# Kernel optimization log

Measured on AMD Instinct MI355X. Metric: run time of the kernel, lower is better.

## Reference

```python
import jax, jax.numpy as jnp
import numpy as np

C = 384
NH = 8        # LocalCrossAttention heads
CA_NH = 2     # inner CrossAttention heads
D_WIN = 6
SIGMA = D_WIN / 2.0
EPS = 1e-6


def _ln(x, g, b):
    mu = jnp.mean(x, axis=-1, keepdims=True)
    var = jnp.mean((x - mu) ** 2, axis=-1, keepdims=True)
    return (x - mu) / jnp.sqrt(var + EPS) * g + b


def _cross_attn(qx, kvx, Wq, Wkv, Wp, bp, nh):
    B, QN, c = qx.shape
    N = kvx.shape[1]
    hd = c // nh
    scale = hd ** -0.5
    qh = (qx @ Wq).reshape(B, QN, nh, hd).transpose(0, 2, 1, 3) * scale  # bhqd
    kvh = (kvx @ Wkv).reshape(B, N, 2, nh, hd).transpose(2, 0, 3, 1, 4)
    k, v = kvh[0], kvh[1]                                               # bhkd
    attn = jax.nn.softmax(jnp.einsum('bhqd,bhkd->bhqk', qh, k), axis=-1)
    x = jnp.einsum('bhqk,bhkd->bhqd', attn, v).transpose(0, 2, 1, 3).reshape(B, QN, c)
    return x @ Wp + bp


def _forward(q, kv, Wq, Wkv, Wproj, bproj, Wp_w, Wp_b, vp_w, vp_b, qpos_w, qpos_b,
             ca1_Wq, ca1_Wkv, ca1_Wproj, ca1_bproj,
             ca2_Wq, ca2_Wkv, ca2_Wproj, ca2_bproj,
             lnq1_g, lnq1_b, lnkv1_g, lnkv1_b, lnq2_g, lnq2_b, lnkv2_g, lnkv2_b, H, W):
    bs, QN, c = q.shape
    N = kv.shape[1]
    hd = c // NH
    scale = hd ** -0.5

    # main q/k/v
    qh = (q @ Wq).reshape(bs, QN, NH, hd).transpose(0, 2, 1, 3) * scale   # [bs,NH,QN,hd]
    kvh = (kv @ Wkv).reshape(bs, N, 2, NH, hd).transpose(2, 0, 3, 1, 4)
    k, v = kvh[0], kvh[1]                                                 # [bs,NH,N,hd]

    # position prediction branch
    q_for_pos = jnp.tile(q, (1, H, 1))                                    # [bs,QN*H,C]
    p = q_for_pos @ qpos_w + qpos_b
    p = _cross_attn(_ln(p, lnq1_g, lnq1_b), _ln(q_for_pos, lnkv1_g, lnkv1_b),
                    ca1_Wq, ca1_Wkv, ca1_Wproj, ca1_bproj, CA_NH)
    p = _cross_attn(_ln(p, lnq2_g, lnq2_b), _ln(kv, lnkv2_g, lnkv2_b),
                    ca2_Wq, ca2_Wkv, ca2_Wproj, ca2_bproj, CA_NH)
    p_t = jax.nn.sigmoid(jnp.tanh(p @ Wp_w + Wp_b) @ vp_w + vp_b) * W     # [bs,QN*H,1]

    # Gaussian window over W columns, broadcast over heads
    idx = jnp.arange(W, dtype=q.dtype)                                    # [W]
    gauss = jnp.exp(-((idx[None, :] - p_t) ** 2) / (2.0 * SIGMA ** 2))    # [bs,QN*H,W]
    gauss = gauss[:, None]                                                # [bs,1,QN*H,W]

    attn = jnp.einsum('bhqd,bhkd->bhqk', qh, k)                           # [bs,NH,QN,N]
    attn = attn.reshape(bs, NH, QN * H, W) * gauss
    attn = attn.reshape(bs, NH, QN, N)
    attn = jax.nn.softmax(attn, axis=-1)

    x = jnp.einsum('bhqk,bhkd->bhqd', attn, v).transpose(0, 2, 1, 3).reshape(bs, QN, c)
    return x @ Wproj + bproj


def setup_inputs() -> dict:
    key = jax.random.key(0)
    ks = jax.random.split(key, 16)
    s = 0.05
    d = {
        'q': jax.random.normal(ks[0], (32, 64, C), jnp.float32),
        'kv': jax.random.normal(ks[1], (32, 1024, C), jnp.float32),
        'Wq': jax.random.normal(ks[2], (C, C), jnp.float32) * s,
        'Wkv': jax.random.normal(ks[3], (C, 2 * C), jnp.float32) * s,
        'Wproj': jax.random.normal(ks[4], (C, C), jnp.float32) * s,
        'bproj': jnp.zeros((C,), jnp.float32),
        'Wp_w': jax.random.normal(ks[5], (C, C), jnp.float32) * s,
        'Wp_b': jnp.zeros((C,), jnp.float32),
        'vp_w': jax.random.normal(ks[6], (C, 1), jnp.float32) * s,
        'vp_b': jnp.zeros((1,), jnp.float32),
        'qpos_w': jax.random.normal(ks[7], (C, C), jnp.float32) * s,
        'qpos_b': jnp.zeros((C,), jnp.float32),
        'ca1_Wq': jax.random.normal(ks[8], (C, C), jnp.float32) * s,
        'ca1_Wkv': jax.random.normal(ks[9], (C, 2 * C), jnp.float32) * s,
        'ca1_Wproj': jax.random.normal(ks[10], (C, C), jnp.float32) * s,
        'ca1_bproj': jnp.zeros((C,), jnp.float32),
        'ca2_Wq': jax.random.normal(ks[11], (C, C), jnp.float32) * s,
        'ca2_Wkv': jax.random.normal(ks[12], (C, 2 * C), jnp.float32) * s,
        'ca2_Wproj': jax.random.normal(ks[13], (C, C), jnp.float32) * s,
        'ca2_bproj': jnp.zeros((C,), jnp.float32),
        'lnq1_g': jnp.ones((C,), jnp.float32), 'lnq1_b': jnp.zeros((C,), jnp.float32),
        'lnkv1_g': jnp.ones((C,), jnp.float32), 'lnkv1_b': jnp.zeros((C,), jnp.float32),
        'lnq2_g': jnp.ones((C,), jnp.float32), 'lnq2_b': jnp.zeros((C,), jnp.float32),
        'lnkv2_g': jnp.ones((C,), jnp.float32), 'lnkv2_b': jnp.zeros((C,), jnp.float32),
        'H': 8,
        'W': 128,
    }
    return d


def reference(q, kv, Wq, Wkv, Wproj, bproj, Wp_w, Wp_b, vp_w, vp_b, qpos_w, qpos_b,
              ca1_Wq, ca1_Wkv, ca1_Wproj, ca1_bproj,
              ca2_Wq, ca2_Wkv, ca2_Wproj, ca2_bproj,
              lnq1_g, lnq1_b, lnkv1_g, lnkv1_b, lnq2_g, lnq2_b, lnkv2_g, lnkv2_b, H, W):
    return _forward(q, kv, Wq, Wkv, Wproj, bproj, Wp_w, Wp_b, vp_w, vp_b, qpos_w, qpos_b,
                    ca1_Wq, ca1_Wkv, ca1_Wproj, ca1_bproj,
                    ca2_Wq, ca2_Wkv, ca2_Wproj, ca2_bproj,
                    lnq1_g, lnq1_b, lnkv1_g, lnkv1_b, lnq2_g, lnq2_b, lnkv2_g, lnkv2_b, H, W)
```

## Files before the change

### kernel.cpp

```cpp
#include <hip/hip_runtime.h>
#include <math.h>

#define MFMA __builtin_amdgcn_mfma_f32_16x16x32_bf16
typedef __attribute__((ext_vector_type(8))) short bf16x8;
typedef __attribute__((ext_vector_type(4))) float f32x4;
typedef __attribute__((ext_vector_type(4))) unsigned short us4;
typedef unsigned short ushort_t;

__device__ __forceinline__ unsigned short tbf_hi(float x) {
    return (unsigned short)(__float_as_uint(x) >> 16);
}
__device__ __forceinline__ unsigned short tbf_lo(float x) {
    unsigned u = __float_as_uint(x);
    float r = x - __uint_as_float(u & 0xFFFF0000u);
    return (unsigned short)(__float_as_uint(r) >> 16);
}
__device__ __forceinline__ unsigned packhi(unsigned u0, unsigned u1) {
#if __has_builtin(__builtin_amdgcn_perm)
    return __builtin_amdgcn_perm(u1, u0, 0x07060302u);
#else
    return (u1 & 0xFFFF0000u) | (u0 >> 16);
#endif
}
__device__ __forceinline__ void tsplit8(const float* v, unsigned* hw, unsigned* lw) {
#pragma unroll
    for (int t = 0; t < 4; ++t) {
        unsigned u0 = __float_as_uint(v[2 * t]);
        unsigned u1 = __float_as_uint(v[2 * t + 1]);
        float r0 = v[2 * t]     - __uint_as_float(u0 & 0xFFFF0000u);
        float r1 = v[2 * t + 1] - __uint_as_float(u1 & 0xFFFF0000u);
        hw[t] = packhi(u0, u1);
        lw[t] = packhi(__float_as_uint(r0), __float_as_uint(r1));
    }
}

#if __has_builtin(__builtin_amdgcn_global_load_lds)
#define HAVE_GLDS 1
__device__ __forceinline__ void gld16(const ushort_t* g, ushort_t* l) {
    __builtin_amdgcn_global_load_lds(
        (const __attribute__((address_space(1))) unsigned int*)g,
        (__attribute__((address_space(3))) unsigned int*)l, 16, 0, 0);
}
#else
#define HAVE_GLDS 0
#endif

__global__ __launch_bounds__(256) void ln_stats_kernel(
    const float* __restrict__ src, float* __restrict__ mu,
    float* __restrict__ rs, int rows) {
    int row = blockIdx.x * 4 + (threadIdx.x >> 6);
    int lane = threadIdx.x & 63;
    if (row >= rows) return;
    const float* p = src + (size_t)row * 384;
    float s = 0.f, sq = 0.f;
#pragma unroll
    for (int i = 0; i < 6; ++i) {
        float v = p[lane + 64 * i];
        s += v; sq += v * v;
    }
#pragma unroll
    for (int off = 32; off > 0; off >>= 1) {
        s += __shfl_down(s, off);
        sq += __shfl_down(sq, off);
    }
    if (lane == 0) {
        float m = s / 384.f;
        float var = sq / 384.f - m * m;
        mu[row] = m;
        rs[row] = rsqrtf(var + 1e-6f);
    }
}

__global__ __launch_bounds__(256) void lnsplit_kernel(
    const float* __restrict__ src, float* __restrict__ mu,
    float* __restrict__ rs, ushort_t* __restrict__ dh,
    ushort_t* __restrict__ dl, int rows) {
    int row = blockIdx.x * 4 + (threadIdx.x >> 6);
    int lane = threadIdx.x & 63;
    if (row >= rows) return;
    const float* p = src + (size_t)row * 384;
    float v[6];
    float s = 0.f, sq = 0.f;
#pragma unroll
    for (int i = 0; i < 6; ++i) {
        v[i] = p[lane + 64 * i];
        s += v[i]; sq += v[i] * v[i];
    }
#pragma unroll
    for (int i = 0; i < 6; ++i) {
        dh[(size_t)row * 384 + lane + 64 * i] = tbf_hi(v[i]);
        dl[(size_t)row * 384 + lane + 64 * i] = tbf_lo(v[i]);
    }
#pragma unroll
    for (int off = 32; off > 0; off >>= 1) {
        s += __shfl_down(s, off);
        sq += __shfl_down(sq, off);
    }
    if (lane == 0) {
        float m = s / 384.f;
        float var = sq / 384.f - m * m;
        mu[row] = m;
        rs[row] = rsqrtf(var + 1e-6f);
    }
}

struct WprepTab {
    const float* src[10]; const float* g[10];
    ushort_t* dh[10]; ushort_t* dl[10];
    float scale[10]; int N[10];
};
__global__ __launch_bounds__(256) void wprep_all(WprepTab t) {
    int e = blockIdx.y;
    int N = t.N[e];
    int idx = blockIdx.x * 256 + threadIdx.x;
    if (idx >= N * 384) return;
    int n = idx / 384, k = idx % 384;
    float x = t.src[e][(size_t)k * N + n] * t.scale[e];
    if (t.g[e]) x *= t.g[e][k];
    t.dh[e][idx] = tbf_hi(x);
    t.dl[e][idx] = tbf_lo(x);
}

struct CmcbTab {
    const float* src[5]; const float* g[5]; const float* lb[5]; const float* badd[5];
    float* cm[5]; float* cb[5]; float scale[5]; int N[5];
};
__global__ __launch_bounds__(256) void cmcb_all(CmcbTab t) {
    int e = blockIdx.y;
    int N = t.N[e];
    int c = blockIdx.x * 4 + (threadIdx.x >> 6);
    int lane = threadIdx.x & 63;
    if (c >= N) return;
    float s1 = 0.f, s2 = 0.f;
    const float* gp = t.g[e];
#pragma unroll
    for (int i = 0; i < 6; ++i) {
        int k = lane + 64 * i;
        float w = t.src[e][(size_t)k * N + c];
        if (gp) s1 += gp[k] * w;
        s2 += t.lb[e][k] * w;
    }
#pragma unroll
    for (int off = 32; off > 0; off >>= 1) {
        s1 += __shfl_down(s1, off);
        s2 += __shfl_down(s2, off);
    }
    if (lane == 0) {
        if (t.cm[e]) t.cm[e][c] = -t.scale[e] * s1;
        float v = t.scale[e] * s2;
        if (t.badd[e]) v += t.badd[e][c];
        t.cb[e][c] = v;
    }
}

struct Slot {
    const float* bias; const float* cm; const float* cb;
    float* f32o; ushort_t* oh; ushort_t* ol;
    int mode; int kvsh;
};
struct GemmCfg { const float* muA; const float* rsA; Slot s[4]; };

template <int TM, int TN, int ASPLIT, int XSWZ>
__global__ __launch_bounds__(256) void gemm_k(
    const float* __restrict__ Af,
    const ushort_t* __restrict__ Ah, const ushort_t* __restrict__ Al,
    const ushort_t* __restrict__ Bh, const ushort_t* __restrict__ Bl,
    GemmCfg cfg) {
    constexpr int MI = TM / 64;
    constexpr int NI = TN / 16;
    constexpr int AR = TM / 32, BR = TN / 32;
    __shared__ __align__(16) ushort_t Alds[2][TM * 64];
    __shared__ __align__(16) ushort_t Blds[2][TN * 64];
    int bx = blockIdx.x, by = blockIdx.y;
    if (XSWZ) {
        int gx = gridDim.x;
        int nwg = gx * gridDim.y;
        int lin = by * gx + bx;
        int cpx = nwg >> 3;
        lin = (lin & 7) * cpx + (lin >> 3);
        by = lin / gx;
        bx = lin - by * gx;
    }
    int m0 = by * TM, n0 = bx * TN;
    int tid = threadIdx.x;
    int w = tid >> 6, lane = tid & 63;
    int j = lane & 15, kg = lane >> 4;
    int srow = tid >> 3, sk16 = tid & 7;
    f32x4 acc[MI][NI];
#pragma unroll
    for (int mi = 0; mi < MI; ++mi)
#pragma unroll
        for (int ni = 0; ni < NI; ++ni)
#pragma unroll
            for (int r = 0; r < 4; ++r) acc[mi][ni][r] = 0.f;

    for (int ks = 0; ks < 6; ++ks) {
        __syncthreads();
#if HAVE_GLDS
        if (ASPLIT) {
#pragma unroll
            for (int i = 0; i < TM / 32; ++i) {
                int lrow = w * (TM / 4) + i * 8 + (lane >> 3);
                int cc = (lane & 7) ^ (lrow & 7);
                size_t ga = (size_t)(m0 + lrow) * 384 + ks * 64 + cc * 8;
                gld16(Ah + ga, &Alds[0][(w * (TM / 4) + i * 8) * 64]);
                gld16(Al + ga, &Alds[1][(w * (TM / 4) + i * 8) * 64]);
            }
#pragma unroll
            for (int i = 0; i < TN / 32; ++i) {
                int lrow = w * (TN / 4) + i * 8 + (lane >> 3);
                int cc = (lane & 7) ^ (lrow & 7);
                size_t gb = (size_t)(n0 + lrow) * 384 + ks * 64 + cc * 8;
                gld16(Bh + gb, &Blds[0][(w * (TN / 4) + i * 8) * 64]);
                gld16(Bl + gb, &Blds[1][(w * (TN / 4) + i * 8) * 64]);
            }
        } else
#endif
        {
            int kbase = ks * 64 + sk16 * 8;
#pragma unroll
            for (int rnd = 0; rnd < AR; ++rnd) {
                int row = srow + rnd * 32;
                int off = (row << 6) + ((sk16 ^ (row & 7)) << 3);
                if (ASPLIT) {
                    size_t ga = (size_t)(m0 + row) * 384 + kbase;
                    *(bf16x8*)&Alds[0][off] = *(const bf16x8*)(Ah + ga);
                    *(bf16x8*)&Alds[1][off] = *(const bf16x8*)(Al + ga);
                } else {
                    const float* ap = Af + (size_t)(m0 + row) * 384 + kbase;
                    float v[8];
                    *(float4*)v = *(const float4*)ap;
                    *(float4*)(v + 4) = *(const float4*)(ap + 4);
                    unsigned hw[4], lw[4];
                    tsplit8(v, hw, lw);
                    *(uint4*)&Alds[0][off] = *(uint4*)hw;
                    *(uint4*)&Alds[1][off] = *(uint4*)lw;
                }
            }
#pragma unroll
            for (int rnd = 0; rnd < BR; ++rnd) {
                int row = srow + rnd * 32;
                int off = (row << 6) + ((sk16 ^ (row & 7)) << 3);
                size_t gb = (size_t)(n0 + row) * 384 + kbase;
                *(bf16x8*)&Blds[0][off] = *(const bf16x8*)(Bh + gb);
                *(bf16x8*)&Blds[1][off] = *(const bf16x8*)(Bl + gb);
            }
        }
        __syncthreads();
#pragma unroll
        for (int kf = 0; kf < 2; ++kf) {
            bf16x8 afh[MI], afl[MI], bfh[NI], bfl[NI];
#pragma unroll
            for (int mi = 0; mi < MI; ++mi) {
                int row = w * (TM / 4) + mi * 16 + j;
                int off = (row << 6) + ((((kf << 2) | kg) ^ (row & 7)) << 3);
                afh[mi] = *(const bf16x8*)&Alds[0][off];
                afl[mi] = *(const bf16x8*)&Alds[1][off];
            }
#pragma unroll
            for (int ni = 0; ni < NI; ++ni) {
                int col = ni * 16 + j;
                int off = (col << 6) + ((((kf << 2) | kg) ^ (col & 7)) << 3);
                bfh[ni] = *(const bf16x8*)&Blds[0][off];
                bfl[ni] = *(const bf16x8*)&Blds[1][off];
            }
#pragma unroll
            for (int mi = 0; mi < MI; ++mi)
#pragma unroll
                for (int ni = 0; ni < NI; ++ni) {
                    acc[mi][ni] = MFMA(afh[mi], bfh[ni], acc[mi][ni], 0, 0, 0);
                    acc[mi][ni] = MFMA(afh[mi], bfl[ni], acc[mi][ni], 0, 0, 0);
                    acc[mi][ni] = MFMA(afl[mi], bfh[ni], acc[mi][ni], 0, 0, 0);
                }
        }
    }
    int slot = n0 / 384;
    Slot sl = cfg.s[slot];
    int cb0 = n0 % 384;
#pragma unroll
    for (int mi = 0; mi < MI; ++mi)
#pragma unroll
        for (int ni = 0; ni < NI; ++ni)
#pragma unroll
            for (int r = 0; r < 4; ++r) {
                int row = m0 + w * (TM / 4) + mi * 16 + kg * 4 + r;
                int c2 = cb0 + ni * 16 + j;
                float v = acc[mi][ni][r];
                if (sl.cm) {
                    float rss = cfg.rsA[row];
                    v = rss * v + rss * cfg.muA[row] * sl.cm[c2] + sl.cb[c2];
                }
                if (sl.bias) v += sl.bias[c2];
                if (sl.mode == 0) {
                    sl.f32o[(size_t)row * 384 + c2] = v;
                } else if (sl.mode == 1) {
                    sl.f32o[(size_t)row * 384 + c2] = tanhf(v);
                } else if (sl.mode == 2) {
                    sl.oh[(size_t)row * 384 + c2] = tbf_hi(v);
                    sl.ol[(size_t)row * 384 + c2] = tbf_lo(v);
                } else if (sl.mode == 4) {
                    size_t o = (size_t)c2 * 384 + row;
                    sl.oh[o] = tbf_hi(v);
                    sl.ol[o] = tbf_lo(v);
                } else {
                    int bb = row >> sl.kvsh;
                    int key = row & ((1 << sl.kvsh) - 1);
                    size_t o = (((size_t)bb * 384 + c2) << sl.kvsh) + key;
                    sl.oh[o] = tbf_hi(v);
                    sl.ol[o] = tbf_lo(v);
                }
            }
}

template <int XSWZ>
__global__ __launch_bounds__(512, 4) void gemm_big(
    const ushort_t* __restrict__ Ah, const ushort_t* __restrict__ Al,
    const ushort_t* __restrict__ Bh, const ushort_t* __restrict__ Bl,
    GemmCfg cfg) {
    __shared__ __align__(16) ushort_t Alds[2][128 * 64];
    __shared__ __align__(16) ushort_t Blds[2][128 * 64];
    int bx = blockIdx.x, by = blockIdx.y;
    if (XSWZ) {
        int gx = gridDim.x;
        int nwg = gx * gridDim.y;
        int lin = by * gx + bx;
        int cpx = nwg >> 3;
        lin = (lin & 7) * cpx + (lin >> 3);
        by = lin / gx;
        bx = lin - by * gx;
    }
    int m0 = by * 128, n0 = bx * 128;
    int tid = threadIdx.x;
    int w = tid >> 6, lane = tid & 63;
    int wm = w >> 2, wn = w & 3;
    int j = lane & 15, kg = lane >> 4;
    f32x4 acc[4][2];
#pragma unroll
    for (int mi = 0; mi < 4; ++mi)
#pragma unroll
        for (int ni = 0; ni < 2; ++ni)
#pragma unroll
            for (int r = 0; r < 4; ++r) acc[mi][ni][r] = 0.f;

    for (int ks = 0; ks < 6; ++ks) {
        __syncthreads();
#pragma unroll
        for (int i = 0; i < 2; ++i) {
            int cbase = (i * 8 + w) * 64;
            int chunk = cbase + lane;
            int lrow = chunk >> 3;
            int cc = (chunk & 7) ^ (lrow & 7);
            size_t ga = (size_t)(m0 + lrow) * 384 + ks * 64 + cc * 8;
            size_t gb = (size_t)(n0 + lrow) * 384 + ks * 64 + cc * 8;
#if HAVE_GLDS
            gld16(Ah + ga, &Alds[0][cbase * 8]);
            gld16(Al + ga, &Alds[1][cbase * 8]);
            gld16(Bh + gb, &Blds[0][cbase * 8]);
            gld16(Bl + gb, &Blds[1][cbase * 8]);
#else
            *(bf16x8*)&Alds[0][chunk * 8] = *(const bf16x8*)(Ah + ga);
            *(bf16x8*)&Alds[1][chunk * 8] = *(const bf16x8*)(Al + ga);
            *(bf16x8*)&Blds[0][chunk * 8] = *(const bf16x8*)(Bh + gb);
            *(bf16x8*)&Blds[1][chunk * 8] = *(const bf16x8*)(Bl + gb);
#endif
        }
        __syncthreads();
#pragma unroll
        for (int kf = 0; kf < 2; ++kf) {
            bf16x8 afh[4], afl[4], bfh[2], bfl[2];
#pragma unroll
            for (int mi = 0; mi < 4; ++mi) {
                int row = wm * 64 + mi * 16 + j;
                int off = (row << 6) + ((((kf << 2) | kg) ^ (row & 7)) << 3);
                afh[mi] = *(const bf16x8*)&Alds[0][off];
                afl[mi] = *(const bf16x8*)&Alds[1][off];
            }
#pragma unroll
            for (int ni = 0; ni < 2; ++ni) {
                int col = wn * 32 + ni * 16 + j;
                int off = (col << 6) + ((((kf << 2) | kg) ^ (col & 7)) << 3);
                bfh[ni] = *(const bf16x8*)&Blds[0][off];
                bfl[ni] = *(const bf16x8*)&Blds[1][off];
            }
#pragma unroll
            for (int mi = 0; mi < 4; ++mi)
#pragma unroll
                for (int ni = 0; ni < 2; ++ni) {
                    acc[mi][ni] = MFMA(afh[mi], bfh[ni], acc[mi][ni], 0, 0, 0);
                    acc[mi][ni] = MFMA(afh[mi], bfl[ni], acc[mi][ni], 0, 0, 0);
                    acc[mi][ni] = MFMA(afl[mi], bfh[ni], acc[mi][ni], 0, 0, 0);
                }
        }
    }
    int slot = n0 / 384;
    Slot sl = cfg.s[slot];
    int cb0 = n0 % 384;
#pragma unroll
    for (int mi = 0; mi < 4; ++mi)
#pragma unroll
        for (int ni = 0; ni < 2; ++ni) {
            int row0 = m0 + wm * 64 + mi * 16 + kg * 4;
            int c2 = cb0 + wn * 32 + ni * 16 + j;
            float v[4];
#pragma unroll
            for (int r = 0; r < 4; ++r) {
                float x = acc[mi][ni][r];
                if (sl.cm) {
                    float rss = cfg.rsA[row0 + r];
                    x = rss * x + rss * cfg.muA[row0 + r] * sl.cm[c2] + sl.cb[c2];
                }
                v[r] = x;
            }
            if (sl.mode == 2) {
#pragma unroll
                for (int r = 0; r < 4; ++r) {
                    sl.oh[(size_t)(row0 + r) * 384 + c2] = tbf_hi(v[r]);
                    sl.ol[(size_t)(row0 + r) * 384 + c2] = tbf_lo(v[r]);
                }
            } else {
                int bb = row0 >> sl.kvsh;
                int key = row0 & ((1 << sl.kvsh) - 1);
                size_t o = (((size_t)bb * 384 + c2) << sl.kvsh) + key;
                us4 h4, l4;
#pragma unroll
                for (int r = 0; r < 4; ++r) { h4[r] = tbf_hi(v[r]); l4[r] = tbf_lo(v[r]); }
                *(us4*)(sl.oh + o) = h4;
                *(us4*)(sl.ol + o) = l4;
            }
        }
}

template <int HD, int DPAD, int NW, int GAUSS, int FINAL>
__global__ __launch_bounds__(64 * NW) void attn_k(
    const ushort_t* __restrict__ Qh, const ushort_t* __restrict__ Ql,
    const ushort_t* __restrict__ Kh, const ushort_t* __restrict__ Kl,
    const ushort_t* __restrict__ Vth, const ushort_t* __restrict__ Vtl,
    const float* __restrict__ PT,
    ushort_t* __restrict__ Xh, ushort_t* __restrict__ Xl,
    float* __restrict__ Opart, float* __restrict__ ML,
    int kvsh, int nch, int NS, int nh) {
    constexpr int KS = DPAD / 32;
    constexpr int NSUB = HD / 16;
    constexpr int C8 = DPAD / 8;
    constexpr int NT = 64 * NW;
    __shared__ __align__(16) ushort_t Ksh[2][32][DPAD + 8];
    __shared__ __align__(16) ushort_t Vsh[2][HD][40];
    __shared__ __align__(16) ushort_t Psh[NW][2][16][40];
    __shared__ float ptbl[GAUSS ? 64 : 1];
    int b = blockIdx.z, h = blockIdx.y, chunk = blockIdx.x;
    int tid = threadIdx.x;
    int w = tid >> 6, lane = tid & 63;
    int l15 = lane & 15, kg = lane >> 4;

    bf16x8 qf[2][KS];
    {
        size_t qa = (size_t)(b * 64 + w * 16 + l15) * 384 + h * HD + kg * 8;
#pragma unroll
        for (int ks = 0; ks < KS; ++ks) {
            if (ks * 32 + kg * 8 < HD) {
                qf[0][ks] = *(const bf16x8*)(Qh + qa + ks * 32);
                qf[1][ks] = *(const bf16x8*)(Ql + qa + ks * 32);
            } else {
                qf[0][ks] = bf16x8{};
                qf[1][ks] = bf16x8{};
            }
        }
    }
    if (GAUSS) {
        if (tid < 64) ptbl[tid] = PT[b * 64 + tid];
    }
    f32x4 oacc[NSUB];
#pragma unroll
    for (int ns = 0; ns < NSUB; ++ns)
#pragma unroll
        for (int r = 0; r < 4; ++r) oacc[ns][r] = 0.f;
    float m_run[4], l_run[4];
#pragma unroll
    for (int r = 0; r < 4; ++r) { m_run[r] = -1e30f; l_run[r] = 0.f; }

    int kbase0 = chunk * nch;
    for (int t = 0; t < nch; t += 32) {
        int n0 = kbase0 + t;
        __syncthreads();
        for (int i = tid; i < 2 * 32 * C8; i += NT) {
            int hl = i / (32 * C8);
            int rem = i - hl * 32 * C8;
            int key = rem / C8, c = rem % C8;
            bf16x8 v;
            if (c * 8 < HD) {
                const ushort_t* src = (hl ? Kl : Kh) +
                    ((size_t)((b << kvsh) + n0 + key)) * 384 + h * HD + c * 8;
                v = *(const bf16x8*)src;
            } else {
                v = bf16x8{};
            }
            *(bf16x8*)&Ksh[hl][key][c * 8] = v;
        }
        for (int i = tid; i < 2 * HD * 4; i += NT) {
            int hl = i / (HD * 4);
            int rem = i - hl * HD * 4;
            int dim = rem >> 2, c = rem & 3;
            const ushort_t* src = (hl ? Vtl : Vth) +
                (((size_t)(b * 384 + h * HD + dim)) << kvsh) + n0 + c * 8;
            *(bf16x8*)&Vsh[hl][dim][c * 8] = *(const bf16x8*)src;
        }
        __syncthreads();

        f32x4 shh[2], slh[2], shl[2];
#pragma unroll
        for (int sub = 0; sub < 2; ++sub)
#pragma unroll
            for (int r = 0; r < 4; ++r) { shh[sub][r] = 0.f; slh[sub][r] = 0.f; shl[sub][r] = 0.f; }
#pragma unroll
        for (int sub = 0; sub < 2; ++sub)
#pragma unroll
            for (int ks = 0; ks < KS; ++ks) {
                bf16x8 kh8 = *(const bf16x8*)&Ksh[0][sub * 16 + l15][ks * 32 + kg * 8];
                bf16x8 kl8 = *(const bf16x8*)&Ksh[1][sub * 16 + l15][ks * 32 + kg * 8];
                shh[sub] = MFMA(qf[0][ks], kh8, shh[sub], 0, 0, 0);
                slh[sub] = MFMA(qf[1][ks], kh8, slh[sub], 0, 0, 0);
                shl[sub] = MFMA(qf[0][ks], kl8, shl[sub], 0, 0, 0);
            }
        f32x4 s[2];
#pragma unroll
        for (int sub = 0; sub < 2; ++sub)
#pragma unroll
            for (int r = 0; r < 4; ++r)
                s[sub][r] = shh[sub][r] + slh[sub][r] + shl[sub][r];
        if (GAUSS) {
            int win = n0 >> 7;
#pragma unroll
            for (int sub = 0; sub < 2; ++sub) {
                float wpos = (float)((n0 + sub * 16 + l15) & 127);
#pragma unroll
                for (int r = 0; r < 4; ++r) {
                    float ptv = ptbl[((w * 16 + kg * 4 + r) * 8 + win) & 63];
                    float d = wpos - ptv;
                    s[sub][r] *= __expf(d * d * (-1.0f / 18.0f));
                }
            }
        }
#pragma unroll
        for (int r = 0; r < 4; ++r) {
            float v = fmaxf(s[0][r], s[1][r]);
            v = fmaxf(v, __shfl_xor(v, 1));
            v = fmaxf(v, __shfl_xor(v, 2));
            v = fmaxf(v, __shfl_xor(v, 4));
            v = fmaxf(v, __shfl_xor(v, 8));
            float mnew = fmaxf(m_run[r], v);
            float alpha = __expf(m_run[r] - mnew);
            m_run[r] = mnew;
            float p0 = __expf(s[0][r] - mnew);
            float p1 = __expf(s[1][r] - mnew);
            float ps = p0 + p1;
            ps += __shfl_xor(ps, 1);
            ps += __shfl_xor(ps, 2);
            ps += __shfl_xor(ps, 4);
            ps += __shfl_xor(ps, 8);
            l_run[r] = l_run[r] * alpha + ps;
#pragma unroll
            for (int ns = 0; ns < NSUB; ++ns) oacc[ns][r] *= alpha;
            Psh[w][0][kg * 4 + r][l15] = tbf_hi(p0);
            Psh[w][1][kg * 4 + r][l15] = tbf_lo(p0);
            Psh[w][0][kg * 4 + r][16 + l15] = tbf_hi(p1);
            Psh[w][1][kg * 4 + r][16 + l15] = tbf_lo(p1);
        }
        bf16x8 pfh = *(const bf16x8*)&Psh[w][0][l15][kg * 8];
        bf16x8 pfl = *(const bf16x8*)&Psh[w][1][l15][kg * 8];
#pragma unroll
        for (int ns = 0; ns < NSUB; ++ns) {
            bf16x8 vh8 = *(const bf16x8*)&Vsh[0][ns * 16 + l15][kg * 8];
            bf16x8 vl8 = *(const bf16x8*)&Vsh[1][ns * 16 + l15][kg * 8];
            oacc[ns] = MFMA(pfh, vh8, oacc[ns], 0, 0, 0);
            oacc[ns] = MFMA(pfl, vh8, oacc[ns], 0, 0, 0);
            oacc[ns] = MFMA(pfh, vl8, oacc[ns], 0, 0, 0);
        }
    }
    if (FINAL) {
#pragma unroll
        for (int ns = 0; ns < NSUB; ++ns)
#pragma unroll
            for (int r = 0; r < 4; ++r) {
                float val = oacc[ns][r] / l_run[r];
                size_t o = (size_t)(b * 64 + w * 16 + kg * 4 + r) * 384 +
                           h * HD + ns * 16 + l15;
                Xh[o] = tbf_hi(val);
                Xl[o] = tbf_lo(val);
            }
    } else {
#pragma unroll
        for (int r = 0; r < 4; ++r) {
            int rq = w * 16 + kg * 4 + r;
            size_t Pidx = ((size_t)((b * nh + h) * 64 + rq)) * NS + chunk;
#pragma unroll
            for (int ns = 0; ns < NSUB; ++ns)
                Opart[Pidx * HD + ns * 16 + l15] = oacc[ns][r];
            if (l15 == 0) {
                ML[Pidx * 2] = m_run[r];
                ML[Pidx * 2 + 1] = l_run[r];
            }
        }
    }
}

template <int HD>
__global__ __launch_bounds__(256) void comb_k(
    const float* __restrict__ Opart, const float* __restrict__ ML,
    ushort_t* __restrict__ Xh, ushort_t* __restrict__ Xl,
    int NS, int nh) {
    int gw = blockIdx.x * 4 + (threadIdx.x >> 6);
    int lane = threadIdx.x & 63;
    if (gw >= 2048 * nh) return;
    int r_ = gw / nh, h = gw % nh;
    int b = r_ >> 6, rq = r_ & 63;
    size_t Pb = ((size_t)((b * nh + h) * 64 + rq)) * NS;
    float M = -1e30f;
    for (int c = 0; c < NS; ++c) M = fmaxf(M, ML[(Pb + c) * 2]);
    float wgt[8];
    float L = 0.f;
    for (int c = 0; c < NS; ++c) {
        wgt[c] = __expf(ML[(Pb + c) * 2] - M);
        L += wgt[c] * ML[(Pb + c) * 2 + 1];
    }
    float invL = 1.f / L;
    for (int d = lane; d < HD; d += 64) {
        float o = 0.f;
        for (int c = 0; c < NS; ++c) o += wgt[c] * Opart[(Pb + c) * HD + d];
        o *= invL;
        size_t xo = (size_t)r_ * 384 + h * HD + d;
        Xh[xo] = tbf_hi(o);
        Xl[xo] = tbf_lo(o);
    }
}

__global__ __launch_bounds__(256) void pt_kernel(
    const float* __restrict__ T, const float* __restrict__ vpw,
    const float* __restrict__ vpb, float* __restrict__ pt, int rows) {
    int row = blockIdx.x * 4 + (threadIdx.x >> 6);
    int lane = threadIdx.x & 63;
    if (row >= rows) return;
    const float* p = T + (size_t)row * 384;
    float s = 0.f;
#pragma unroll
    for (int i = 0; i < 6; ++i) s += p[lane + 64 * i] * vpw[lane + 64 * i];
#pragma unroll
    for (int off = 32; off > 0; off >>= 1) s += __shfl_down(s, off);
    if (lane == 0) {
        float x = s + vpb[0];
        pt[row] = 128.f / (1.f + __expf(-x));
    }
}

extern "C" void kernel_launch(void* const* d_in, const int* in_sizes, int n_in,
                              void* d_out, int out_size, void* d_ws, size_t ws_size,
                              hipStream_t stream) {
    const float* q       = (const float*)d_in[0];
    const float* kv      = (const float*)d_in[1];
    const float* Wq      = (const float*)d_in[2];
    const float* Wkv     = (const float*)d_in[3];
    const float* Wproj   = (const float*)d_in[4];
    const float* bproj   = (const float*)d_in[5];
    const float* Wp_w    = (const float*)d_in[6];
    const float* Wp_b    = (const float*)d_in[7];
    const float* vp_w    = (const float*)d_in[8];
    const float* vp_b    = (const float*)d_in[9];
    const float* qpos_w  = (const float*)d_in[10];
    const float* qpos_b  = (const float*)d_in[11];
    const float* ca1_Wq  = (const float*)d_in[12];
    const float* ca1_Wkv = (const float*)d_in[13];
    const float* ca1_Wp  = (const float*)d_in[14];
    const float* ca1_bp  = (const float*)d_in[15];
    const float* ca2_Wq  = (const float*)d_in[16];
    const float* ca2_Wkv = (const float*)d_in[17];
    const float* ca2_Wp  = (const float*)d_in[18];
    const float* ca2_bp  = (const float*)d_in[19];
    const float* lnq1_g  = (const float*)d_in[20];
    const float* lnq1_b  = (const float*)d_in[21];
    const float* lnkv1_g = (const float*)d_in[22];
    const float* lnkv1_b = (const float*)d_in[23];
    const float* lnq2_g  = (const float*)d_in[24];
    const float* lnq2_b  = (const float*)d_in[25];
    const float* lnkv2_g = (const float*)d_in[26];
    const float* lnkv2_b = (const float*)d_in[27];
    float* out = (float*)d_out;

    const float SC_CA = 0.07216878364870323f;
    const float SC_MA = 0.14433756729740643f;

    float* F = (float*)d_ws;
    float* R0 = F;    F += 786432;
    float* R1 = F;    F += 786432;
    float* MUq = F;   F += 2048;
    float* RSq = F;   F += 2048;
    float* MUkv = F;  F += 32768;
    float* RSkv = F;  F += 32768;
    float* MUpa = F;  F += 2048;
    float* RSpa = F;  F += 2048;
    float* MUpb = F;  F += 2048;
    float* RSpb = F;  F += 2048;
    float* PTb = F;   F += 2048;
    float* CM = F;    F += 2304;
    float* CB = F;    F += 2688;
    float* OP = F;    F += 6291456;
    float* MLb = F;   F += 262144;
    ushort_t* U = (ushort_t*)F;
    ushort_t* WB1h = U; U += 589824;
    ushort_t* WB1l = U; U += 589824;
    ushort_t* WB5h = U; U += 589824;
    ushort_t* WB5l = U; U += 589824;
    ushort_t* W2h = U;  U += 147456;
    ushort_t* W2l = U;  U += 147456;
    ushort_t* W3h = U;  U += 147456;
    ushort_t* W3l = U;  U += 147456;
    ushort_t* W4h = U;  U += 147456;
    ushort_t* W4l = U;  U += 147456;
    ushort_t* W67h = U; U += 147456;
    ushort_t* W67l = U; U += 147456;
    ushort_t* W7h = U;  U += 147456;
    ushort_t* W7l = U;  U += 147456;
    ushort_t* W10h = U; U += 147456;
    ushort_t* W10l = U; U += 147456;
    ushort_t* Qch = U;  U += 786432;
    ushort_t* Qcl = U;  U += 786432;
    ushort_t* Qmh = U;  U += 786432;
    ushort_t* Qml = U;  U += 786432;
    ushort_t* Xh = U;   U += 786432;
    ushort_t* Xl = U;   U += 786432;
    ushort_t* K1h = U;  U += 786432;
    ushort_t* K1l = U;  U += 786432;
    ushort_t* V1h = U;  U += 786432;
    ushort_t* V1l = U;  U += 786432;
    ushort_t* K2h = U;  U += 12582912;
    ushort_t* K2l = U;  U += 12582912;
    ushort_t* V2h = U;  U += 12582912;
    ushort_t* V2l = U;  U += 12582912;
    ushort_t* Qsh = U;  U += 786432;
    ushort_t* Qsl = U;  U += 786432;
    ushort_t* KVsh = U; U += 12582912;
    ushort_t* KVsl = U; U += 12582912;
    ushort_t* Kmh = K2h;
    ushort_t* Kml = K2l;
    ushort_t* Vmh = V2h;
    ushort_t* Vml = V2l;

    dim3 blk(256);

    lnsplit_kernel<<<512, blk, 0, stream>>>(q, MUq, RSq, Qsh, Qsl, 2048);
    lnsplit_kernel<<<8192, blk, 0, stream>>>(kv, MUkv, RSkv, KVsh, KVsl, 32768);

    WprepTab wt{};
    const float* wsrc[10] = {qpos_w, ca1_Wkv, Wq, ca2_Wkv, Wkv,
                             ca1_Wq, ca1_Wp, ca2_Wq, Wp_w, Wproj};
    const float* wg[10] = {nullptr, lnkv1_g, nullptr, lnkv2_g, nullptr,
                           lnq1_g, nullptr, lnq2_g, nullptr, nullptr};
    ushort_t* wdh[10] = {WB1h, WB1h + 384 * 384, WB1h + 1152 * 384,
                         WB5h, WB5h + 768 * 384, W2h, W3h, W4h, W7h, W10h};
    ushort_t* wdl[10] = {WB1l, WB1l + 384 * 384, WB1l + 1152 * 384,
                         WB5l, WB5l + 768 * 384, W2l, W3l, W4l, W7l, W10l};
    float wsc[10] = {1.f, 1.f, SC_MA, 1.f, 1.f, SC_CA, 1.f, SC_CA, 1.f, 1.f};
    int wn[10] = {384, 768, 384, 768, 768, 384, 384, 384, 384, 384};
    for (int i = 0; i < 10; ++i) {
        wt.src[i] = wsrc[i]; wt.g[i] = wg[i]; wt.dh[i] = wdh[i];
        wt.dl[i] = wdl[i]; wt.scale[i] = wsc[i]; wt.N[i] = wn[i];
    }
    wprep_all<<<dim3(1152, 10), blk, 0, stream>>>(wt);

    CmcbTab ct{};
    const float* csrc[5] = {ca1_Wq, ca1_Wkv, ca2_Wq, ca2_Wkv, Wp_w};
    const float* cg[5] = {lnq1_g, lnkv1_g, lnq2_g, lnkv2_g, nullptr};
    const float* cl[5] = {lnq1_b, lnkv1_b, lnq2_b, lnkv2_b, ca2_bp};
    const float* cbad[5] = {nullptr, nullptr, nullptr, nullptr, Wp_b};
    float* ccm[5] = {CM, CM + 384, CM + 1152, CM + 1536, nullptr};
    float* ccb[5] = {CB, CB + 384, CB + 1152, CB + 1536, CB + 2304};
    float csc[5] = {SC_CA, 1.f, SC_CA, 1.f, 1.f};
    int cn[5] = {384, 768, 384, 768, 384};
    for (int i = 0; i < 5; ++i) {
        ct.src[i] = csrc[i]; ct.g[i] = cg[i]; ct.lb[i] = cl[i]; ct.badd[i] = cbad[i];
        ct.cm[i] = ccm[i]; ct.cb[i] = ccb[i]; ct.scale[i] = csc[i]; ct.N[i] = cn[i];
    }
    cmcb_all<<<dim3(192, 5), blk, 0, stream>>>(ct);

    GemmCfg gW{};
    gW.s[0] = {nullptr, nullptr, nullptr, nullptr, W67h, W67l, 4, 0};
    gemm_k<64, 64, 0, 0><<<dim3(6, 6), blk, 0, stream>>>(ca2_Wp, nullptr, nullptr, W7h, W7l, gW);

    GemmCfg g5a{};
    g5a.muA = MUkv; g5a.rsA = RSkv;
    g5a.s[0] = {nullptr, CM + 1536, CB + 1536, nullptr, K2h, K2l, 2, 0};
    g5a.s[1] = {nullptr, CM + 1920, CB + 1920, nullptr, V2h, V2l, 3, 10};
    gemm_big<1><<<dim3(6, 256), dim3(512), 0, stream>>>(KVsh, KVsl, WB5h, WB5l, g5a);

    GemmCfg g1{};
    g1.muA = MUq; g1.rsA = RSq;
    g1.s[0] = {qpos_b, nullptr, nullptr, R0, nullptr, nullptr, 0, 0};
    g1.s[1] = {nullptr, CM + 384, CB + 384, nullptr, K1h, K1l, 2, 0};
    g1.s[2] = {nullptr, CM + 768, CB + 768, nullptr, V1h, V1l, 3, 6};
    g1.s[3] = {nullptr, nullptr, nullptr, nullptr, Qmh, Qml, 2, 0};
    gemm_k<64, 64, 1, 1><<<dim3(24, 32), blk, 0, stream>>>(nullptr, Qsh, Qsl, WB1h, WB1l, g1);

    ln_stats_kernel<<<512, blk, 0, stream>>>(R0, MUpa, RSpa, 2048);

    GemmCfg g2{};
    g2.muA = MUpa; g2.rsA = RSpa;
    g2.s[0] = {nullptr, CM, CB, nullptr, Qch, Qcl, 2, 0};
    gemm_k<64, 64, 0, 0><<<dim3(6, 32), blk, 0, stream>>>(R0, nullptr, nullptr, W2h, W2l, g2);

    attn_k<192, 192, 4, 0, 1><<<dim3(1, 2, 32), blk, 0, stream>>>(
        Qch, Qcl, K1h, K1l, V1h, V1l, nullptr, Xh, Xl, nullptr, nullptr, 6, 64, 1, 2);

    GemmCfg g3{};
    g3.s[0] = {ca1_bp, nullptr, nullptr, R1, nullptr, nullptr, 0, 0};
    gemm_k<64, 64, 1, 0><<<dim3(6, 32), blk, 0, stream>>>(nullptr, Xh, Xl, W3h, W3l, g3);

    ln_stats_kernel<<<512, blk, 0, stream>>>(R1, MUpb, RSpb, 2048);

    GemmCfg g4{};
    g4.muA = MUpb; g4.rsA = RSpb;
    g4.s[0] = {nullptr, CM + 1152, CB + 1152, nullptr, Qch, Qcl, 2, 0};
    gemm_k<64, 64, 0, 0><<<dim3(6, 32), blk, 0, stream>>>(R1, nullptr, nullptr, W4h, W4l, g4);

    attn_k<192, 192, 4, 0, 0><<<dim3(8, 2, 32), blk, 0, stream>>>(
        Qch, Qcl, K2h, K2l, V2h, V2l, nullptr, nullptr, nullptr, OP, MLb, 10, 128, 8, 2);
    comb_k<192><<<1024, blk, 0, stream>>>(OP, MLb, Xh, Xl, 8, 2);

    GemmCfg g67{};
    g67.s[0] = {CB + 2304, nullptr, nullptr, R0, nullptr, nullptr, 1, 0};
    gemm_k<64, 64, 1, 0><<<dim3(6, 32), blk, 0, stream>>>(nullptr, Xh, Xl, W67h, W67l, g67);

    pt_kernel<<<512, blk, 0, stream>>>(R0, vp_w, vp_b, PTb, 2048);

    GemmCfg g5b{};
    g5b.s[0] = {nullptr, nullptr, nullptr, nullptr, Kmh, Kml, 2, 0};
    g5b.s[1] = {nullptr, nullptr, nullptr, nullptr, Vmh, Vml, 3, 10};
    gemm_big<1><<<dim3(6, 256), dim3(512), 0, stream>>>(KVsh, KVsl,
        WB5h + 768 * 384, WB5l + 768 * 384, g5b);

    attn_k<48, 64, 4, 1, 0><<<dim3(8, 8, 32), blk, 0, stream>>>(
        Qmh, Qml, Kmh, Kml, Vmh, Vml, PTb, nullptr, nullptr, OP, MLb, 10, 128, 8, 8);
    comb_k<48><<<4096, blk, 0, stream>>>(OP, MLb, Xh, Xl, 8, 8);

    GemmCfg g10{};
    g10.s[0] = {bproj, nullptr, nullptr, out, nullptr, nullptr, 0, 0};
    gemm_k<64, 64, 1, 0><<<dim3(6, 32), blk, 0, stream>>>(nullptr, Xh, Xl, W10h, W10l, g10);
}
```

Baseline: 451.7 us.

## Stage gemm_big epilogue through LDS for coalesced stores and route g1 to it

```diff
diff --git a/kernel.cpp b/kernel.cpp
--- a/kernel.cpp
+++ b/kernel.cpp
@@ -317,8 +317,11 @@
     const ushort_t* __restrict__ Ah, const ushort_t* __restrict__ Al,
     const ushort_t* __restrict__ Bh, const ushort_t* __restrict__ Bl,
     GemmCfg cfg) {
-    __shared__ __align__(16) ushort_t Alds[2][128 * 64];
-    __shared__ __align__(16) ushort_t Blds[2][128 * 64];
+    __shared__ __align__(16) ushort_t SMEM[32768];
+    ushort_t* const A0 = SMEM;
+    ushort_t* const A1 = SMEM + 8192;
+    ushort_t* const B0 = SMEM + 16384;
+    ushort_t* const B1 = SMEM + 24576;
     int bx = blockIdx.x, by = blockIdx.y;
     if (XSWZ) {
         int gx = gridDim.x;
@@ -353,15 +356,15 @@
             size_t ga = (size_t)(m0 + lrow) * 384 + ks * 64 + cc * 8;
             size_t gb = (size_t)(n0 + lrow) * 384 + ks * 64 + cc * 8;
 #if HAVE_GLDS
-            gld16(Ah + ga, &Alds[0][cbase * 8]);
-            gld16(Al + ga, &Alds[1][cbase * 8]);
-            gld16(Bh + gb, &Blds[0][cbase * 8]);
-            gld16(Bl + gb, &Blds[1][cbase * 8]);
+            gld16(Ah + ga, A0 + cbase * 8);
+            gld16(Al + ga, A1 + cbase * 8);
+            gld16(Bh + gb, B0 + cbase * 8);
+            gld16(Bl + gb, B1 + cbase * 8);
 #else
-            *(bf16x8*)&Alds[0][chunk * 8] = *(const bf16x8*)(Ah + ga);
-            *(bf16x8*)&Alds[1][chunk * 8] = *(const bf16x8*)(Al + ga);
-            *(bf16x8*)&Blds[0][chunk * 8] = *(const bf16x8*)(Bh + gb);
-            *(bf16x8*)&Blds[1][chunk * 8] = *(const bf16x8*)(Bl + gb);
+            *(bf16x8*)(A0 + chunk * 8) = *(const bf16x8*)(Ah + ga);
+            *(bf16x8*)(A1 + chunk * 8) = *(const bf16x8*)(Al + ga);
+            *(bf16x8*)(B0 + chunk * 8) = *(const bf16x8*)(Bh + gb);
+            *(bf16x8*)(B1 + chunk * 8) = *(const bf16x8*)(Bl + gb);
 #endif
         }
         __syncthreads();
@@ -372,15 +375,15 @@
             for (int mi = 0; mi < 4; ++mi) {
                 int row = wm * 64 + mi * 16 + j;
                 int off = (row << 6) + ((((kf << 2) | kg) ^ (row & 7)) << 3);
-                afh[mi] = *(const bf16x8*)&Alds[0][off];
-                afl[mi] = *(const bf16x8*)&Alds[1][off];
+                afh[mi] = *(const bf16x8*)(A0 + off);
+                afl[mi] = *(const bf16x8*)(A1 + off);
             }
 #pragma unroll
             for (int ni = 0; ni < 2; ++ni) {
                 int col = wn * 32 + ni * 16 + j;
                 int off = (col << 6) + ((((kf << 2) | kg) ^ (col & 7)) << 3);
-                bfh[ni] = *(const bf16x8*)&Blds[0][off];
-                bfl[ni] = *(const bf16x8*)&Blds[1][off];
+                bfh[ni] = *(const bf16x8*)(B0 + off);
+                bfl[ni] = *(const bf16x8*)(B1 + off);
             }
 #pragma unroll
             for (int mi = 0; mi < 4; ++mi)
@@ -395,39 +398,84 @@
     int slot = n0 / 384;
     Slot sl = cfg.s[slot];
     int cb0 = n0 % 384;
+
+    if (sl.mode <= 1) {
+#pragma unroll
+        for (int mi = 0; mi < 4; ++mi)
+#pragma unroll
+            for (int ni = 0; ni < 2; ++ni)
+#pragma unroll
+                for (int r = 0; r < 4; ++r) {
+                    int row = m0 + wm * 64 + mi * 16 + kg * 4 + r;
+                    int c2 = cb0 + wn * 32 + ni * 16 + j;
+                    float v = acc[mi][ni][r];
+                    if (sl.cm) {
+                        float rss = cfg.rsA[row];
+                        v = rss * v + rss * cfg.muA[row] * sl.cm[c2] + sl.cb[c2];
+                    }
+                    if (sl.bias) v += sl.bias[c2];
+                    if (sl.mode == 1) v = tanhf(v);
+                    sl.f32o[(size_t)row * 384 + c2] = v;
+                }
+        return;
+    }
+
+    __syncthreads();
 #pragma unroll
     for (int mi = 0; mi < 4; ++mi)
 #pragma unroll
         for (int ni = 0; ni < 2; ++ni) {
-            int row0 = m0 + wm * 64 + mi * 16 + kg * 4;
-            int c2 = cb0 + wn * 32 + ni * 16 + j;
+            int rr0 = wm * 64 + mi * 16 + kg * 4;
+            int c2rel = wn * 32 + ni * 16 + j;
+            int c2 = cb0 + c2rel;
             float v[4];
 #pragma unroll
             for (int r = 0; r < 4; ++r) {
                 float x = acc[mi][ni][r];
                 if (sl.cm) {
-                    float rss = cfg.rsA[row0 + r];
-                    x = rss * x + rss * cfg.muA[row0 + r] * sl.cm[c2] + sl.cb[c2];
+                    float rss = cfg.rsA[m0 + rr0 + r];
+                    x = rss * x + rss * cfg.muA[m0 + rr0 + r] * sl.cm[c2] + sl.cb[c2];
                 }
+                if (sl.bias) x += sl.bias[c2];
                 v[r] = x;
             }
-            if (sl.mode == 2) {
+            if (sl.mode == 3) {
+                int idx = c2rel * 128 + (rr0 ^ ((c2rel & 7) << 3));
+                us4 h4, l4;
+#pragma unroll
+                for (int r = 0; r < 4; ++r) { h4[r] = tbf_hi(v[r]); l4[r] = tbf_lo(v[r]); }
+                *(us4*)&SMEM[idx] = h4;
+                *(us4*)&SMEM[16384 + idx] = l4;
+            } else {
 #pragma unroll
                 for (int r = 0; r < 4; ++r) {
-                    sl.oh[(size_t)(row0 + r) * 384 + c2] = tbf_hi(v[r]);
-                    sl.ol[(size_t)(row0 + r) * 384 + c2] = tbf_lo(v[r]);
+                    int rowrel = rr0 + r;
+                    int idx = rowrel * 128 + (c2rel ^ ((rowrel & 7) << 3));
+                    SMEM[idx] = tbf_hi(v[r]);
+                    SMEM[16384 + idx] = tbf_lo(v[r]);
                 }
-            } else {
-                int bb = row0 >> sl.kvsh;
-                int key = row0 & ((1 << sl.kvsh) - 1);
-                size_t o = (((size_t)bb * 384 + c2) << sl.kvsh) + key;
-                us4 h4, l4;
-#pragma unroll
-                for (int r = 0; r < 4; ++r) { h4[r] = tbf_hi(v[r]); l4[r] = tbf_lo(v[r]); }
-                *(us4*)(sl.oh + o) = h4;
-                *(us4*)(sl.ol + o) = l4;
-            }
-        }
+            }
+        }
+    __syncthreads();
+    int pr = tid >> 2, seg = tid & 3;
+#pragma unroll
+    for (int i = 0; i < 4; ++i) {
+        int off = seg * 32 + i * 8;
+        int idx = pr * 128 + (off ^ ((pr & 7) << 3));
+        bf16x8 hv = *(const bf16x8*)&SMEM[idx];
+        bf16x8 lv = *(const bf16x8*)&SMEM[16384 + idx];
+        size_t o;
+        if (sl.mode == 3) {
+            int keyg = m0 + off;
+            int bb = keyg >> sl.kvsh;
+            int key = keyg & ((1 << sl.kvsh) - 1);
+            o = (((size_t)(bb * 384 + cb0 + pr)) << sl.kvsh) + key;
+        } else {
+            o = (size_t)(m0 + pr) * 384 + cb0 + off;
+        }
+        *(bf16x8*)(sl.oh + o) = hv;
+        *(bf16x8*)(sl.ol + o) = lv;
+    }
 }
 
 template <int HD, int DPAD, int NW, int GAUSS, int FINAL>
@@ -796,7 +844,7 @@
     g1.s[1] = {nullptr, CM + 384, CB + 384, nullptr, K1h, K1l, 2, 0};
     g1.s[2] = {nullptr, CM + 768, CB + 768, nullptr, V1h, V1l, 3, 6};
     g1.s[3] = {nullptr, nullptr, nullptr, nullptr, Qmh, Qml, 2, 0};
-    gemm_k<64, 64, 1, 1><<<dim3(24, 32), blk, 0, stream>>>(nullptr, Qsh, Qsl, WB1h, WB1l, g1);
+    gemm_big<1><<<dim3(12, 16), dim3(512), 0, stream>>>(Qsh, Qsl, WB1h, WB1l, g1);
 
     ln_stats_kernel<<<512, blk, 0, stream>>>(R0, MUpa, RSpa, 2048);
 
```

After: 478.5 us. +5.9%, slower.
